# Kernel tuning notes

Hardware: AMD Instinct MI355X
Metric: run time of the kernel (lower is better)

The kernel has to match this reference:

```python
import jax, jax.numpy as jnp
import numpy as np

N_NODES = 50000
IN_CH = 128
HID = 128
N_EDGES = 800000


def _glorot(key, shape):
    fan_in, fan_out = shape[0], shape[1]
    lim = (6.0 / (fan_in + fan_out)) ** 0.5
    return jax.random.uniform(key, shape, jnp.float32, -lim, lim)


def setup_inputs() -> dict:
    key = jax.random.key(0)
    ks = jax.random.split(key, 8)
    x = jax.random.normal(ks[0], (N_NODES, IN_CH), jnp.float32)
    edge_index = jax.random.randint(ks[1], (2, N_EDGES), 0, N_NODES, jnp.int64)
    return {
        "x": x,
        "edge_index": edge_index,
        # SAGEConv1: lin_l (with bias) applied to mean-aggregated neighbors,
        # lin_r (no bias) applied to root features (PyG defaults, mean aggr)
        "W1l": _glorot(ks[2], (IN_CH, HID)),
        "b1l": jnp.zeros((HID,), jnp.float32),
        "W1r": _glorot(ks[3], (IN_CH, HID)),
        # SAGEConv2
        "W2l": _glorot(ks[4], (HID, HID)),
        "b2l": jnp.zeros((HID,), jnp.float32),
        "W2r": _glorot(ks[5], (HID, HID)),
        # final Linear(hidden, 1)
        "Wout": _glorot(ks[6], (HID, 1)),
        "bout": jnp.zeros((1,), jnp.float32),
    }


def _sage_conv(x, src, dst, Wl, bl, Wr, n_nodes):
    # gather source features along edges, mean-reduce into destinations
    msgs = x[src]                                                # [E, D]
    sums = jax.ops.segment_sum(msgs, dst, num_segments=n_nodes)  # [N, D]
    cnt = jax.ops.segment_sum(jnp.ones((src.shape[0], 1), x.dtype), dst,
                              num_segments=n_nodes)              # [N, 1]
    agg = sums / jnp.maximum(cnt, 1.0)
    return agg @ Wl + bl + x @ Wr


def reference(x, edge_index, W1l, b1l, W1r, W2l, b2l, W2r, Wout, bout):
    src, dst = edge_index[0], edge_index[1]
    n = x.shape[0]
    h = jax.nn.relu(_sage_conv(x, src, dst, W1l, b1l, W1r, n))
    h = jax.nn.relu(_sage_conv(h, src, dst, W2l, b2l, W2r, n))
    return (h @ Wout + bout).squeeze(-1)  # [N]
```

## Files before the change

### kernel.cpp

```cpp
#include <hip/hip_runtime.h>

#define D 128
#define LSTR 132
#define CAP 3072
#define NBLK 256

typedef __attribute__((ext_vector_type(8))) short short8;
typedef __attribute__((ext_vector_type(4))) float f32x4;

static __device__ __forceinline__ unsigned short f2bf(float f) {
    unsigned u = __float_as_uint(f);
    return (unsigned short)((u + 0x7fffu + ((u >> 16) & 1u)) >> 16);
}
static __device__ __forceinline__ float b2f(unsigned short u) {
    return __uint_as_float(((unsigned)u) << 16);
}


__global__ void prep_kernel(const float* __restrict__ x,
                            const float* __restrict__ W1l,
                            const float* __restrict__ W1r,
                            const float* __restrict__ W2l,
                            const float* __restrict__ W2r,
                            unsigned* __restrict__ xb2,
                            unsigned short* __restrict__ Bt1,
                            unsigned short* __restrict__ Bt2, int NX2) {
    const int i = blockIdx.x * blockDim.x + threadIdx.x;
    if (i < NX2) {
        const float2 v = *(const float2*)(x + 2 * (size_t)i);
        xb2[i] = (unsigned)f2bf(v.x) | ((unsigned)f2bf(v.y) << 16);
    } else if (i < NX2 + 2 * 32768) {
        const int j = i - NX2;
        const int which = j >> 15;
        const int jj = j & 32767;
        const int n = jj >> 8;
        const int k = jj & 255;
        const float* Wl = which ? W2l : W1l;
        const float* Wr = which ? W2r : W1r;
        const float w = (k < 128) ? Wl[k * 128 + n] : Wr[(k - 128) * 128 + n];
        (which ? Bt2 : Bt1)[jj] = f2bf(w);
    }
}

__global__ __launch_bounds__(256) void histA_kernel(const int* __restrict__ dst,
                                                    int E, int nbins,
                                                    unsigned* __restrict__ G) {
    __shared__ int h[2048];
    const int t = threadIdx.x;
    for (int i = t; i < nbins; i += 256) h[i] = 0;
    __syncthreads();
    const int per = (E + NBLK - 1) / NBLK;
    const int lo = blockIdx.x * per;
    const int hi = min(lo + per, E);
    for (int i = lo + t; i < hi; i += 256) atomicAdd(&h[dst[i] >> 5], 1);
    __syncthreads();
    for (int i = t; i < nbins; i += 256)
        G[(size_t)i * NBLK + blockIdx.x] = (unsigned)h[i];
}

__global__ __launch_bounds__(256) void scanB_kernel(unsigned* __restrict__ G,
                                                    int nbins,
                                                    int* __restrict__ tot) {
    const int wave = threadIdx.x >> 6;
    const int lane = threadIdx.x & 63;
    const int bin = blockIdx.x * 4 + wave;
    if (bin >= nbins) return;
    unsigned* p = G + (size_t)bin * NBLK + lane * 4;
    uint4 v = *(uint4*)p;
    const unsigned s = v.x + v.y + v.z + v.w;
    unsigned sc = s;
#pragma unroll
    for (int off = 1; off < 64; off <<= 1) {
        const unsigned u = (unsigned)__shfl_up((int)sc, off, 64);
        if (lane >= off) sc += u;
    }
    const unsigned excl = sc - s;
    uint4 w;
    w.x = excl;
    w.y = excl + v.x;
    w.z = excl + v.x + v.y;
    w.w = excl + v.x + v.y + v.z;
    *(uint4*)p = w;
    if (lane == 63) tot[bin] = (int)(excl + s);
}

__global__ __launch_bounds__(1024) void scanC_kernel(
    const int* __restrict__ tot, int nbins, int* __restrict__ tile_base) {
    __shared__ int part[1024];
    const int t = threadIdx.x;
    const int chunk = (nbins + 1023) >> 10;
    const int lo = min(t * chunk, nbins);
    const int hi = min(lo + chunk, nbins);
    int s = 0;
    for (int i = lo; i < hi; ++i) s += tot[i];
    part[t] = s;
    __syncthreads();
    for (int off = 1; off < 1024; off <<= 1) {
        int add = (t >= off) ? part[t - off] : 0;
        __syncthreads();
        part[t] += add;
        __syncthreads();
    }
    int excl = (t == 0) ? 0 : part[t - 1];
    for (int i = lo; i < hi; ++i) {
        tile_base[i] = excl;
        excl += tot[i];
    }
    if (t == 1023) tile_base[nbins] = part[1023];
}

__global__ __launch_bounds__(256) void fillB_kernel(
    const int* __restrict__ src, const int* __restrict__ dst, int E,
    const unsigned* __restrict__ G, const int* __restrict__ tile_base,
    unsigned* __restrict__ csr, int nbins) {
    __shared__ int rank[2048];
    __shared__ int base[2048];
    const int t = threadIdx.x;
    for (int i = t; i < nbins; i += 256) {
        rank[i] = 0;
        base[i] = tile_base[i] + (int)G[(size_t)i * NBLK + blockIdx.x];
    }
    __syncthreads();
    const int per = (E + NBLK - 1) / NBLK;
    const int lo = blockIdx.x * per;
    const int hi = min(lo + per, E);
    for (int i = lo + t; i < hi; i += 256) {
        const int d = dst[i];
        const int bin = d >> 5;
        const int r = atomicAdd(&rank[bin], 1);
        csr[base[bin] + r] = (unsigned)src[i] | ((unsigned)d << 16);
    }
}

template <bool HEAD>
__global__ __launch_bounds__(256) void sage_kernel(
    const unsigned short* __restrict__ xb, const unsigned* __restrict__ csr,
    const int* __restrict__ tile_base,
    const unsigned short* __restrict__ Bt,
    const float* __restrict__ bl, const float* __restrict__ Wout,
    const float* __restrict__ bout, unsigned short* __restrict__ hb_out,
    float* __restrict__ out, int N) {
    __shared__ float aggL[32 * LSTR];
    __shared__ unsigned sortedE[CAP];
    __shared__ int rowcnt[32];
    __shared__ int rowofs[32];
    __shared__ float invL[32];
    __shared__ float redH[64];

    const int b = blockIdx.x;
    const int i0 = b * 32;
    const int t = threadIdx.x;
    const int g = t >> 5;
    const int l = t & 31;
    const int c4 = l << 2;

    const int rs0 = tile_base[b];
    const int re0 = tile_base[b + 1];
    const int nE = re0 - rs0;
    const bool use_sorted = (nE <= CAP);

    for (int i = t; i < 32 * LSTR; i += 256) aggL[i] = 0.f;
    if (t < 32) rowcnt[t] = 0;
    __syncthreads();

    for (int i = t; i < nE; i += 256)
        atomicAdd(&rowcnt[(csr[rs0 + i] >> 16) & 31], 1);
    __syncthreads();

    if (t < 32) {
        const int v = rowcnt[t];
        invL[t] = 1.0f / fmaxf((float)v, 1.0f);
        int s = v;
#pragma unroll
        for (int off = 1; off < 32; off <<= 1) {
            const int u = __shfl_up(s, off, 32);
            if (l >= off) s += u;
        }
        rowofs[t] = s - v;
    }
    __syncthreads();

    if (use_sorted) {
        for (int i = t; i < nE; i += 256) {
            const unsigned p = csr[rs0 + i];
            const int k = atomicAdd(&rowofs[(p >> 16) & 31], 1);
            sortedE[k] = p;
        }
    }
    __syncthreads();

    int e = (nE * g) >> 3;
    const int ee = (nE * (g + 1)) >> 3;

    auto getp = [&](int idx) -> unsigned {
        return use_sorted ? sortedE[idx] : csr[rs0 + idx];
    };

    float4 acc = make_float4(0.f, 0.f, 0.f, 0.f);
    int cur = (e < ee) ? (int)(getp(e) >> 16) - i0 : -1;

    auto load4 = [&](unsigned p) -> float4 {
        const ushort4 u =
            *(const ushort4*)(xb + (size_t)(p & 0xffffu) * D + c4);
        float4 v;
        v.x = b2f(u.x); v.y = b2f(u.y); v.z = b2f(u.z); v.w = b2f(u.w);
        return v;
    };
    auto step = [&](unsigned p, const float4& v) {
        const int r = (int)(p >> 16) - i0;
        if (r != cur) {
            float* q = aggL + cur * LSTR + c4;
            atomicAdd(q + 0, acc.x);
            atomicAdd(q + 1, acc.y);
            atomicAdd(q + 2, acc.z);
            atomicAdd(q + 3, acc.w);
            acc = make_float4(0.f, 0.f, 0.f, 0.f);
            cur = r;
        }
        acc.x += v.x; acc.y += v.y; acc.z += v.z; acc.w += v.w;
    };

    while (e + 8 <= ee) {
        const unsigned p0 = getp(e + 0), p1 = getp(e + 1);
        const unsigned p2 = getp(e + 2), p3 = getp(e + 3);
        const unsigned p4 = getp(e + 4), p5 = getp(e + 5);
        const unsigned p6 = getp(e + 6), p7 = getp(e + 7);
        const float4 v0 = load4(p0), v1 = load4(p1), v2 = load4(p2),
                     v3 = load4(p3), v4 = load4(p4), v5 = load4(p5),
                     v6 = load4(p6), v7 = load4(p7);
        step(p0, v0); step(p1, v1); step(p2, v2); step(p3, v3);
        step(p4, v4); step(p5, v5); step(p6, v6); step(p7, v7);
        e += 8;
    }
    while (e < ee) {
        const unsigned p = getp(e);
        step(p, load4(p));
        ++e;
    }
    if (cur >= 0) {
        float* q = aggL + cur * LSTR + c4;
        atomicAdd(q + 0, acc.x);
        atomicAdd(q + 1, acc.y);
        atomicAdd(q + 2, acc.z);
        atomicAdd(q + 3, acc.w);
    }
    __syncthreads();

    const int wave = t >> 6;
    const int lane = t & 63;
    const int ln = lane & 15;
    const int quad = lane >> 4;
    const int mtile = wave & 1;
    const int nt0 = (wave >> 1) * 4;
    const int mrow = mtile * 16 + ln;
    const int gmr = i0 + mrow;
    const float inv = invL[mrow];

    f32x4 acc4[4] = {f32x4{0.f, 0.f, 0.f, 0.f}, f32x4{0.f, 0.f, 0.f, 0.f},
                     f32x4{0.f, 0.f, 0.f, 0.f}, f32x4{0.f, 0.f, 0.f, 0.f}};

#pragma unroll
    for (int s = 0; s < 4; ++s) {
        const int kb = s * 32 + quad * 8;
        const float* ap = aggL + mrow * LSTR + kb;
        const float4 fa = *(const float4*)ap;
        const float4 fb = *(const float4*)(ap + 4);
        const short8 aA = {(short)f2bf(fa.x * inv), (short)f2bf(fa.y * inv),
                           (short)f2bf(fa.z * inv), (short)f2bf(fa.w * inv),
                           (short)f2bf(fb.x * inv), (short)f2bf(fb.y * inv),
                           (short)f2bf(fb.z * inv), (short)f2bf(fb.w * inv)};
        short8 aX = {0, 0, 0, 0, 0, 0, 0, 0};
        if (gmr < N) aX = *(const short8*)(xb + (size_t)gmr * D + kb);
#pragma unroll
        for (int nt = 0; nt < 4; ++nt) {
            const int n = (nt0 + nt) * 16 + ln;
            const short8 b1 = *(const short8*)(Bt + n * 256 + kb);
            const short8 b2 = *(const short8*)(Bt + n * 256 + 128 + kb);
            acc4[nt] = __builtin_amdgcn_mfma_f32_16x16x32_bf16(aA, b1, acc4[nt],
                                                               0, 0, 0);
            acc4[nt] = __builtin_amdgcn_mfma_f32_16x16x32_bf16(aX, b2, acc4[nt],
                                                               0, 0, 0);
        }
    }

    float biasv[4], woutv[4];
#pragma unroll
    for (int nt = 0; nt < 4; ++nt) {
        const int col = (nt0 + nt) * 16 + ln;
        biasv[nt] = bl[col];
        if (HEAD) woutv[nt] = Wout[col];
    }

    if (!HEAD) {
#pragma unroll
        for (int r = 0; r < 4; ++r) {
            const int gr = i0 + mtile * 16 + quad * 4 + r;
            if (gr < N) {
#pragma unroll
                for (int nt = 0; nt < 4; ++nt) {
                    const int col = (nt0 + nt) * 16 + ln;
                    const float v = fmaxf(acc4[nt][r] + biasv[nt], 0.f);
                    hb_out[(size_t)gr * D + col] = f2bf(v);
                }
            }
        }
    } else {
        const float b0 = bout[0];
#pragma unroll
        for (int r = 0; r < 4; ++r) {
            const int row = mtile * 16 + quad * 4 + r;
            float p = 0.f;
#pragma unroll
            for (int nt = 0; nt < 4; ++nt) {
                const float v = fmaxf(acc4[nt][r] + biasv[nt], 0.f);
                p += v * woutv[nt];
            }
            p += __shfl_xor(p, 1);
            p += __shfl_xor(p, 2);
            p += __shfl_xor(p, 4);
            p += __shfl_xor(p, 8);
            if (ln == 0) redH[row * 2 + (wave >> 1)] = p;
        }
        __syncthreads();
        if (t < 32) {
            const int gr = i0 + t;
            if (gr < N) out[gr] = redH[t * 2] + redH[t * 2 + 1] + b0;
        }
    }
}

extern "C" void kernel_launch(void* const* d_in, const int* in_sizes, int n_in,
                              void* d_out, int out_size, void* d_ws,
                              size_t ws_size, hipStream_t stream) {
    const float* x = (const float*)d_in[0];
    const int* ei = (const int*)d_in[1];
    const float* W1l = (const float*)d_in[2];
    const float* b1l = (const float*)d_in[3];
    const float* W1r = (const float*)d_in[4];
    const float* W2l = (const float*)d_in[5];
    const float* b2l = (const float*)d_in[6];
    const float* W2r = (const float*)d_in[7];
    const float* Wout = (const float*)d_in[8];
    const float* bout = (const float*)d_in[9];

    const int N = in_sizes[0] / D;
    const int E = in_sizes[1] / 2;
    const int* src = ei;
    const int* dst = ei + E;

    const int nbins = (N + 31) / 32;
    const size_t Epad = (size_t)((E + 255) & ~255);

    int* tot = (int*)d_ws;
    int* tile_base = tot + 2048;
    unsigned* G = (unsigned*)(tile_base + 2052);
    unsigned* csr = G + (size_t)2048 * NBLK;
    unsigned short* xb = (unsigned short*)(csr + Epad);
    unsigned short* hb = xb + (size_t)N * D;
    unsigned short* Bt1 = hb + (size_t)N * D;
    unsigned short* Bt2 = Bt1 + 128 * 256;
    float* out = (float*)d_out;

    const int NX2 = N * D / 2;
    const int prep_total = NX2 + 2 * 32768;

    prep_kernel<<<(prep_total + 255) / 256, 256, 0, stream>>>(
        x, W1l, W1r, W2l, W2r, (unsigned*)xb, Bt1, Bt2, NX2);
    histA_kernel<<<NBLK, 256, 0, stream>>>(dst, E, nbins, G);
    scanB_kernel<<<(nbins + 3) / 4, 256, 0, stream>>>(G, nbins, tot);
    scanC_kernel<<<1, 1024, 0, stream>>>(tot, nbins, tile_base);
    fillB_kernel<<<NBLK, 256, 0, stream>>>(src, dst, E, G, tile_base, csr,
                                           nbins);

    sage_kernel<false><<<nbins, 256, 0, stream>>>(
        xb, csr, tile_base, Bt1, b1l, nullptr, nullptr, hb, nullptr, N);
    sage_kernel<true><<<nbins, 256, 0, stream>>>(
        hb, csr, tile_base, Bt2, b2l, Wout, bout, nullptr, out, N);
}
```

Measured before the change: 269.2 us.

## Hoist per-tile edge sort into separate kernel and fuse prep with histogram

Moves the per-tile row counting and counting sort of CSR edges out of both sage kernels into a new sortT kernel that sorts csr in place and writes per-row inverse degrees to global memory, so the sort runs once instead of twice. The sage kernels now read csr directly from global and load inverse degrees, which drops the large sortedE shared buffer and may improve occupancy. The prep and histogram kernels are merged into one launch, with block ranges split by role. The cost is an extra kernel launch plus a global read-write pass over csr.

```diff
diff --git a/kernel.cpp b/kernel.cpp
--- a/kernel.cpp
+++ b/kernel.cpp
@@ -17,15 +17,28 @@
 }
 
 
-__global__ void prep_kernel(const float* __restrict__ x,
-                            const float* __restrict__ W1l,
-                            const float* __restrict__ W1r,
-                            const float* __restrict__ W2l,
-                            const float* __restrict__ W2r,
-                            unsigned* __restrict__ xb2,
-                            unsigned short* __restrict__ Bt1,
-                            unsigned short* __restrict__ Bt2, int NX2) {
-    const int i = blockIdx.x * blockDim.x + threadIdx.x;
+__global__ __launch_bounds__(256) void prep_hist_kernel(
+    const float* __restrict__ x, const float* __restrict__ W1l,
+    const float* __restrict__ W1r, const float* __restrict__ W2l,
+    const float* __restrict__ W2r, unsigned* __restrict__ xb2,
+    unsigned short* __restrict__ Bt1, unsigned short* __restrict__ Bt2,
+    int NX2, const int* __restrict__ dst, int E, int nbins,
+    unsigned* __restrict__ G) {
+    const int t = threadIdx.x;
+    if (blockIdx.x < NBLK) {
+        __shared__ int h[2048];
+        for (int i = t; i < nbins; i += 256) h[i] = 0;
+        __syncthreads();
+        const int per = (E + NBLK - 1) / NBLK;
+        const int lo = blockIdx.x * per;
+        const int hi = min(lo + per, E);
+        for (int i = lo + t; i < hi; i += 256) atomicAdd(&h[dst[i] >> 5], 1);
+        __syncthreads();
+        for (int i = t; i < nbins; i += 256)
+            G[(size_t)i * NBLK + blockIdx.x] = (unsigned)h[i];
+        return;
+    }
+    const int i = (blockIdx.x - NBLK) * 256 + t;
     if (i < NX2) {
         const float2 v = *(const float2*)(x + 2 * (size_t)i);
         xb2[i] = (unsigned)f2bf(v.x) | ((unsigned)f2bf(v.y) << 16);
@@ -42,22 +55,6 @@
     }
 }
 
-__global__ __launch_bounds__(256) void histA_kernel(const int* __restrict__ dst,
-                                                    int E, int nbins,
-                                                    unsigned* __restrict__ G) {
-    __shared__ int h[2048];
-    const int t = threadIdx.x;
-    for (int i = t; i < nbins; i += 256) h[i] = 0;
-    __syncthreads();
-    const int per = (E + NBLK - 1) / NBLK;
-    const int lo = blockIdx.x * per;
-    const int hi = min(lo + per, E);
-    for (int i = lo + t; i < hi; i += 256) atomicAdd(&h[dst[i] >> 5], 1);
-    __syncthreads();
-    for (int i = t; i < nbins; i += 256)
-        G[(size_t)i * NBLK + blockIdx.x] = (unsigned)h[i];
-}
-
 __global__ __launch_bounds__(256) void scanB_kernel(unsigned* __restrict__ G,
                                                     int nbins,
                                                     int* __restrict__ tot) {
@@ -132,18 +129,58 @@
     }
 }
 
+__global__ __launch_bounds__(256) void sortT_kernel(unsigned* __restrict__ csr,
+                                                    const int* __restrict__
+                                                        tile_base,
+                                                    float* __restrict__ invL_g,
+                                                    int N) {
+    __shared__ unsigned sortedE[CAP];
+    __shared__ int rowcnt[32];
+    __shared__ int rowofs[32];
+    const int b = blockIdx.x;
+    const int i0 = b * 32;
+    const int t = threadIdx.x;
+    const int rs0 = tile_base[b];
+    const int re0 = tile_base[b + 1];
+    const int nE = re0 - rs0;
+
+    if (t < 32) rowcnt[t] = 0;
+    __syncthreads();
+    for (int i = t; i < nE; i += 256)
+        atomicAdd(&rowcnt[(csr[rs0 + i] >> 16) & 31], 1);
+    __syncthreads();
+    if (t < 32) {
+        const int v = rowcnt[t];
+        if (i0 + t < N) invL_g[i0 + t] = 1.0f / fmaxf((float)v, 1.0f);
+        int s = v;
+#pragma unroll
+        for (int off = 1; off < 32; off <<= 1) {
+            const int u = __shfl_up(s, off, 32);
+            if ((t & 31) >= off) s += u;
+        }
+        rowofs[t] = s - v;
+    }
+    __syncthreads();
+    if (nE <= CAP) {
+        for (int i = t; i < nE; i += 256) {
+            const unsigned p = csr[rs0 + i];
+            const int k = atomicAdd(&rowofs[(p >> 16) & 31], 1);
+            sortedE[k] = p;
+        }
+        __syncthreads();
+        for (int i = t; i < nE; i += 256) csr[rs0 + i] = sortedE[i];
+    }
+}
+
 template <bool HEAD>
 __global__ __launch_bounds__(256) void sage_kernel(
     const unsigned short* __restrict__ xb, const unsigned* __restrict__ csr,
-    const int* __restrict__ tile_base,
+    const int* __restrict__ tile_base, const float* __restrict__ invL_g,
     const unsigned short* __restrict__ Bt,
     const float* __restrict__ bl, const float* __restrict__ Wout,
     const float* __restrict__ bout, unsigned short* __restrict__ hb_out,
     float* __restrict__ out, int N) {
     __shared__ float aggL[32 * LSTR];
-    __shared__ unsigned sortedE[CAP];
-    __shared__ int rowcnt[32];
-    __shared__ int rowofs[32];
     __shared__ float invL[32];
     __shared__ float redH[64];
 
@@ -154,50 +191,18 @@
     const int l = t & 31;
     const int c4 = l << 2;
 
+    for (int i = t; i < 32 * LSTR; i += 256) aggL[i] = 0.f;
+    if (t < 32) invL[t] = (i0 + t < N) ? invL_g[i0 + t] : 1.0f;
+    __syncthreads();
+
     const int rs0 = tile_base[b];
     const int re0 = tile_base[b + 1];
     const int nE = re0 - rs0;
-    const bool use_sorted = (nE <= CAP);
-
-    for (int i = t; i < 32 * LSTR; i += 256) aggL[i] = 0.f;
-    if (t < 32) rowcnt[t] = 0;
-    __syncthreads();
-
-    for (int i = t; i < nE; i += 256)
-        atomicAdd(&rowcnt[(csr[rs0 + i] >> 16) & 31], 1);
-    __syncthreads();
-
-    if (t < 32) {
-        const int v = rowcnt[t];
-        invL[t] = 1.0f / fmaxf((float)v, 1.0f);
-        int s = v;
-#pragma unroll
-        for (int off = 1; off < 32; off <<= 1) {
-            const int u = __shfl_up(s, off, 32);
-            if (l >= off) s += u;
-        }
-        rowofs[t] = s - v;
-    }
-    __syncthreads();
-
-    if (use_sorted) {
-        for (int i = t; i < nE; i += 256) {
-            const unsigned p = csr[rs0 + i];
-            const int k = atomicAdd(&rowofs[(p >> 16) & 31], 1);
-            sortedE[k] = p;
-        }
-    }
-    __syncthreads();
-
-    int e = (nE * g) >> 3;
-    const int ee = (nE * (g + 1)) >> 3;
-
-    auto getp = [&](int idx) -> unsigned {
-        return use_sorted ? sortedE[idx] : csr[rs0 + idx];
-    };
+    int e = rs0 + ((nE * g) >> 3);
+    const int ee = rs0 + ((nE * (g + 1)) >> 3);
 
     float4 acc = make_float4(0.f, 0.f, 0.f, 0.f);
-    int cur = (e < ee) ? (int)(getp(e) >> 16) - i0 : -1;
+    int cur = (e < ee) ? (int)(csr[e] >> 16) - i0 : -1;
 
     auto load4 = [&](unsigned p) -> float4 {
         const ushort4 u =
@@ -221,10 +226,10 @@
     };
 
     while (e + 8 <= ee) {
-        const unsigned p0 = getp(e + 0), p1 = getp(e + 1);
-        const unsigned p2 = getp(e + 2), p3 = getp(e + 3);
-        const unsigned p4 = getp(e + 4), p5 = getp(e + 5);
-        const unsigned p6 = getp(e + 6), p7 = getp(e + 7);
+        const unsigned p0 = csr[e + 0], p1 = csr[e + 1];
+        const unsigned p2 = csr[e + 2], p3 = csr[e + 3];
+        const unsigned p4 = csr[e + 4], p5 = csr[e + 5];
+        const unsigned p6 = csr[e + 6], p7 = csr[e + 7];
         const float4 v0 = load4(p0), v1 = load4(p1), v2 = load4(p2),
                      v3 = load4(p3), v4 = load4(p4), v5 = load4(p5),
                      v6 = load4(p6), v7 = load4(p7);
@@ -233,7 +238,7 @@
         e += 8;
     }
     while (e < ee) {
-        const unsigned p = getp(e);
+        const unsigned p = csr[e];
         step(p, load4(p));
         ++e;
     }
@@ -349,11 +354,13 @@
     const int* dst = ei + E;
 
     const int nbins = (N + 31) / 32;
+    const size_t Npad = (size_t)((N + 255) & ~255);
     const size_t Epad = (size_t)((E + 255) & ~255);
 
     int* tot = (int*)d_ws;
     int* tile_base = tot + 2048;
-    unsigned* G = (unsigned*)(tile_base + 2052);
+    float* invL_g = (float*)(tile_base + 2052);
+    unsigned* G = (unsigned*)(invL_g + Npad);
     unsigned* csr = G + (size_t)2048 * NBLK;
     unsigned short* xb = (unsigned short*)(csr + Epad);
     unsigned short* hb = xb + (size_t)N * D;
@@ -362,18 +369,18 @@
     float* out = (float*)d_out;
 
     const int NX2 = N * D / 2;
-    const int prep_total = NX2 + 2 * 32768;
-
-    prep_kernel<<<(prep_total + 255) / 256, 256, 0, stream>>>(
-        x, W1l, W1r, W2l, W2r, (unsigned*)xb, Bt1, Bt2, NX2);
-    histA_kernel<<<NBLK, 256, 0, stream>>>(dst, E, nbins, G);
+    const int prep_blocks = (NX2 + 2 * 32768 + 255) / 256;
+
+    prep_hist_kernel<<<NBLK + prep_blocks, 256, 0, stream>>>(
+        x, W1l, W1r, W2l, W2r, (unsigned*)xb, Bt1, Bt2, NX2, dst, E, nbins, G);
     scanB_kernel<<<(nbins + 3) / 4, 256, 0, stream>>>(G, nbins, tot);
     scanC_kernel<<<1, 1024, 0, stream>>>(tot, nbins, tile_base);
     fillB_kernel<<<NBLK, 256, 0, stream>>>(src, dst, E, G, tile_base, csr,
                                            nbins);
+    sortT_kernel<<<nbins, 256, 0, stream>>>(csr, tile_base, invL_g, N);
 
     sage_kernel<false><<<nbins, 256, 0, stream>>>(
-        xb, csr, tile_base, Bt1, b1l, nullptr, nullptr, hb, nullptr, N);
+        xb, csr, tile_base, invL_g, Bt1, b1l, nullptr, nullptr, hb, nullptr, N);
     sage_kernel<true><<<nbins, 256, 0, stream>>>(
-        hb, csr, tile_base, Bt2, b2l, Wout, bout, nullptr, out, N);
-}
+        hb, csr, tile_base, invL_g, Bt2, b2l, Wout, bout, nullptr, out, N);
+}
```

Measured after the change: 258.4 us. -4.0%, faster.
